# Kernel optimization log

Measured on AMD Instinct MI355X. Metric: run time of the kernel, lower is better.

Reference implementation:

```python
import jax, jax.numpy as jnp
import numpy as np

B, N, K = 8, 2048, 32
WIDTH = 20.0      # histogram bin width in degrees
NUM_BINS = 9
EPS = 1e-12       # F.normalize eps


def _knn_idx(pts, k):
    """pts: (B,N,3) -> (B,N,k) indices of k nearest neighbors (incl. self).
    Matches dgcnn.pytorch knn: topk of negative squared distance."""
    d2 = jnp.sum(pts * pts, axis=-1)                       # (B,N)
    neg = 2.0 * jnp.einsum('bnd,bmd->bnm', pts, pts) - d2[:, :, None] - d2[:, None, :]
    _, idx = jax.lax.top_k(neg, k)                         # (B,N,k)
    return idx


def _gather_nn(feat, idx):
    """feat: (B,N,C), idx: (B,N,k) -> (B,N,k,C) per-batch gather."""
    return jax.vmap(lambda f, i: f[i])(feat, idx)


def setup_inputs() -> dict:
    key = jax.random.key(0)
    x = jax.random.normal(key, (B, 3, N), dtype=jnp.float32)
    return {"x": x, "k": K}


def reference(x, k):
    """Faithful JAX port of compute_hog_1x1. x: (B,3,N) -> (B,18,N)."""
    b, _, n = x.shape
    pts = jnp.transpose(x, (0, 2, 1))                      # (B,N,3)
    idx = _knn_idx(pts, k)                                 # (B,N,k)

    x_nn = _gather_nn(pts, idx)                            # (B,N,k,3)
    centered = x_nn - x_nn.mean(axis=2, keepdims=True)

    # Batched SVD; the original detaches (numpy round-trip) -> stop_gradient.
    _, s, vh = jnp.linalg.svd(centered, full_matrices=False)  # s:(B,N,3) vh:(B,N,3,3)
    vh = jax.lax.stop_gradient(vh)
    s = jax.lax.stop_gradient(jnp.sqrt(s))
    gradients = vh[:, :, 0]                                # (B,N,3) principal direction
    magnitudes = s[:, :, 0:1]                              # (B,N,1)

    g_nn = _gather_nn(gradients, idx)                      # (B,N,k,3)
    m_nn = _gather_nn(magnitudes, idx)                     # (B,N,k,1)

    rad2deg = 180.0 / np.pi
    zenith = jnp.arccos(g_nn[..., 2]) * rad2deg            # (B,N,k)
    azimuth = jnp.arctan(g_nn[..., 1] / g_nn[..., 0]) * rad2deg
    # .int() cast in torch truncates toward zero
    ang = jnp.stack([zenith, azimuth], axis=-1).astype(jnp.int32).astype(x.dtype)
    ang = jnp.where(ang < 0, ang + 180.0, ang)             # (B,N,k,2)

    bins = jnp.floor(ang / WIDTH - 0.5) % NUM_BINS         # (B,N,k,2) float
    first_centers = WIDTH * ((bins + 1.0) % NUM_BINS + 0.5)
    first_votes = m_nn * ((first_centers - ang) % 180.0) / WIDTH
    second_centers = WIDTH * (bins + 0.5)
    second_votes = m_nn * ((ang - second_centers) % 180.0) / WIDTH

    bi = bins.astype(jnp.int32)                            # (B,N,k,2)
    oh1 = jax.nn.one_hot(bi, NUM_BINS, dtype=x.dtype)      # (B,N,k,2,9)
    oh2 = jax.nn.one_hot((bi + 1) % NUM_BINS, NUM_BINS, dtype=x.dtype)
    # histogram[:, :, c] += first where bins==c; histogram[:, :, (c+1)%9] += second
    hist = (jnp.einsum('bnkc,bnkcq->bnqc', first_votes, oh1)
            + jnp.einsum('bnkc,bnkcq->bnqc', second_votes, oh2))  # (B,N,9,2)

    # F.normalize(p=2, dim=2)
    norm = jnp.sqrt(jnp.sum(hist * hist, axis=2, keepdims=True))
    hist = hist / jnp.maximum(norm, EPS)

    # torch .view(B, -1, N): flat row-major reinterpret -> (B,18,N)
    return hist.reshape(b, 2 * NUM_BINS, n)
```

## Files before the change

### kernel.cpp

```cpp
#include <hip/hip_runtime.h>
#include <math.h>

#define BB 8
#define NN 2048
#define KK 32

__device__ __forceinline__ float fadd(float a, float b){ return __fadd_rn(a, b); }
__device__ __forceinline__ float fsub(float a, float b){ return __fsub_rn(a, b); }
__device__ __forceinline__ float fmul(float a, float b){ return __fmul_rn(a, b); }
__device__ __forceinline__ float fdiv(float a, float b){ return __fdiv_rn(a, b); }
__device__ __forceinline__ float fsqrtf32(float a){ return __fsqrt_rn(a); }

__device__ float slapy2f(float x, float y) {
    float xa = fabsf(x), ya = fabsf(y);
    float w = fmaxf(xa, ya), z = fminf(xa, ya);
    if (z == 0.0f) return w;
    float q = fdiv(z, w);
    return fmul(w, fsqrtf32(fmaf(q, q, 1.0f)));
}

__device__ void slartgf(float f, float g, float& c, float& s, float& r) {
    if (g == 0.0f) { c = 1.0f; s = 0.0f; r = f; }
    else if (f == 0.0f) { c = 0.0f; s = copysignf(1.0f, g); r = fabsf(g); }
    else {
        float d = fsqrtf32(fmaf(f, f, fmul(g, g)));
        c = fdiv(fabsf(f), d);
        r = copysignf(d, f);
        s = fdiv(g, r);
    }
}

__device__ void slas2f(float f, float g, float h, float& ssmin, float& ssmax) {
    float fa = fabsf(f), ga = fabsf(g), ha = fabsf(h);
    float fhmn = fminf(fa, ha), fhmx = fmaxf(fa, ha);
    if (fhmn == 0.0f) {
        ssmin = 0.0f;
        if (fhmx == 0.0f) ssmax = ga;
        else {
            float mx = fmaxf(fhmx, ga), mn = fminf(fhmx, ga);
            float q = fdiv(mn, mx);
            ssmax = fmul(mx, fsqrtf32(fmaf(q, q, 1.0f)));
        }
    } else {
        if (ga < fhmx) {
            float as = fadd(1.0f, fdiv(fhmn, fhmx));
            float at = fdiv(fsub(fhmx, fhmn), fhmx);
            float q = fdiv(ga, fhmx); float au = fmul(q, q);
            float c = fdiv(2.0f, fadd(fsqrtf32(fmaf(as, as, au)),
                                      fsqrtf32(fmaf(at, at, au))));
            ssmin = fmul(fhmn, c); ssmax = fdiv(fhmx, c);
        } else {
            float au = fdiv(fhmx, ga);
            if (au == 0.0f) { ssmin = fdiv(fmul(fhmn, fhmx), ga); ssmax = ga; }
            else {
                float as = fadd(1.0f, fdiv(fhmn, fhmx));
                float at = fdiv(fsub(fhmx, fhmn), fhmx);
                float t1 = fmul(as, au), t2 = fmul(at, au);
                float c = fdiv(1.0f, fadd(fsqrtf32(fmaf(t1, t1, 1.0f)),
                                          fsqrtf32(fmaf(t2, t2, 1.0f))));
                ssmin = fmul(fmul(fhmn, c), au); ssmin = fadd(ssmin, ssmin);
                ssmax = fdiv(ga, fadd(c, c));
            }
        }
    }
}

__device__ void slasv2f(float f, float g, float h,
                        float& ssmin, float& ssmax,
                        float& snr, float& csr, float& snl, float& csl) {
    const float eps = 5.9604644775390625e-08f;
    float ft = f, fa = fabsf(f), ht = h, ha = fabsf(h);
    int pmax = 1;
    bool swp = (ha > fa);
    if (swp) { pmax = 3; float t = ft; ft = ht; ht = t; t = fa; fa = ha; ha = t; }
    float gt = g, ga = fabsf(gt);
    float clt = 0.f, crt = 0.f, slt = 0.f, srt = 0.f;
    if (ga == 0.0f) {
        ssmin = ha; ssmax = fa; clt = 1.0f; crt = 1.0f; slt = 0.0f; srt = 0.0f;
    } else {
        bool gasmal = true;
        if (ga > fa) {
            pmax = 2;
            if (fdiv(fa, ga) < eps) {
                gasmal = false;
                ssmax = ga;
                ssmin = (ha > 1.0f) ? fdiv(fa, fdiv(ga, ha)) : fmul(fdiv(fa, ga), ha);
                clt = 1.0f; slt = fdiv(ht, gt); srt = 1.0f; crt = fdiv(ft, gt);
            }
        }
        if (gasmal) {
            float dd = fsub(fa, ha);
            float l = (dd == fa) ? 1.0f : fdiv(dd, fa);
            float mm = fdiv(gt, ft);
            float t = fsub(2.0f, l);
            float m2 = fmul(mm, mm);
            float s = fsqrtf32(fmaf(t, t, m2));
            float r = (l == 0.0f) ? fabsf(mm) : fsqrtf32(fmaf(l, l, m2));
            float a = fmul(0.5f, fadd(s, r));
            ssmin = fdiv(ha, a);
            ssmax = fmul(fa, a);
            if (m2 == 0.0f) {
                t = (l == 0.0f) ? fmul(copysignf(2.0f, ft), copysignf(1.0f, gt))
                                : fadd(fdiv(gt, copysignf(dd, ft)), fdiv(mm, t));
            } else {
                t = fmul(fadd(fdiv(mm, fadd(s, t)), fdiv(mm, fadd(r, l))), fadd(1.0f, a));
            }
            float l2 = fsqrtf32(fmaf(t, t, 4.0f));
            crt = fdiv(2.0f, l2); srt = fdiv(t, l2);
            clt = fdiv(fmaf(srt, mm, crt), a);
            slt = fdiv(fmul(fdiv(ht, ft), srt), a);
        }
    }
    if (swp) { csl = srt; snl = crt; csr = slt; snr = clt; }
    else     { csl = clt; snl = slt; csr = crt; snr = srt; }
    float tsign = 0.0f;
    if (pmax == 1) tsign = fmul(fmul(copysignf(1.f, csr), copysignf(1.f, csl)), copysignf(1.f, f));
    if (pmax == 2) tsign = fmul(fmul(copysignf(1.f, snr), copysignf(1.f, csl)), copysignf(1.f, g));
    if (pmax == 3) tsign = fmul(fmul(copysignf(1.f, snr), copysignf(1.f, snl)), copysignf(1.f, h));
    ssmax = copysignf(fabsf(ssmax), tsign);
    ssmin = copysignf(fabsf(ssmin), fmul(tsign, fmul(copysignf(1.f, f), copysignf(1.f, h))));
}

__device__ __forceinline__ void rot_rowsf(float vt[4][4], int lo, int hi, float cc, float ss) {
    #pragma unroll
    for (int c = 1; c <= 3; ++c) {
        float t = vt[hi][c];
        vt[hi][c] = fmaf(cc, t, -fmul(ss, vt[lo][c]));
        vt[lo][c] = fmaf(ss, t, fmul(cc, vt[lo][c]));
    }
}

__device__ void bdsqr3f(float* d, float* e, float vt[4][4]) {
    const float eps  = 5.9604644775390625e-08f;
    const float unfl = 1.1754943508222875e-38f;
    const int n = 3;
    const float tol = fmul(10.0f, eps);
    float thresh;
    {
        float sminoa = fabsf(d[1]);
        if (sminoa != 0.0f) {
            float mu = sminoa;
            for (int i = 2; i <= n; ++i) {
                mu = fmul(fabsf(d[i]), fdiv(mu, fadd(mu, fabsf(e[i - 1]))));
                sminoa = fminf(sminoa, mu);
                if (sminoa == 0.0f) break;
            }
        }
        sminoa = fdiv(sminoa, fsqrtf32(3.0f));
        thresh = fmaxf(fmul(tol, sminoa), fmul(54.0f, unfl));
    }
    int m = n, iter = 0, oldll = -1, oldm = -1, idir = 0;
    float sminl = 0.0f;
    while (m > 1) {
        if (iter > 54) break;
        float smax = fabsf(d[m]);
        int ll = 0; bool split = false;
        for (int lll = 1; lll <= m - 1; ++lll) {
            int l2 = m - lll;
            float abss = fabsf(d[l2]), abse = fabsf(e[l2]);
            if (abse <= thresh) { ll = l2; split = true; break; }
            smax = fmaxf(smax, fmaxf(abss, abse));
        }
        if (split) {
            e[ll] = 0.0f;
            if (ll == m - 1) { m = m - 1; continue; }
            ll = ll + 1;
        } else ll = 1;
        if (ll == m - 1) {
            float sigmn, sigmx, sinr, cosr, sinl, cosl;
            slasv2f(d[m - 1], e[m - 1], d[m], sigmn, sigmx, sinr, cosr, sinl, cosl);
            d[m - 1] = sigmx; e[m - 1] = 0.0f; d[m] = sigmn;
            #pragma unroll
            for (int c = 1; c <= 3; ++c) {
                float t = fmaf(cosr, vt[m - 1][c], fmul(sinr, vt[m][c]));
                vt[m][c] = fmaf(cosr, vt[m][c], -fmul(sinr, vt[m - 1][c]));
                vt[m - 1][c] = t;
            }
            m -= 2; continue;
        }
        if (ll > oldm || m < oldll)
            idir = (fabsf(d[ll]) >= fabsf(d[m])) ? 1 : 2;
        bool deflated = false;
        if (idir == 1) {
            if (fabsf(e[m - 1]) <= fmul(tol, fabsf(d[m]))) { e[m - 1] = 0.0f; continue; }
            float mu = fabsf(d[ll]); sminl = mu;
            for (int lll = ll; lll <= m - 1; ++lll) {
                if (fabsf(e[lll]) <= fmul(tol, mu)) { e[lll] = 0.0f; deflated = true; break; }
                mu = fmul(fabsf(d[lll + 1]), fdiv(mu, fadd(mu, fabsf(e[lll]))));
                sminl = fminf(sminl, mu);
            }
        } else {
            if (fabsf(e[ll]) <= fmul(tol, fabsf(d[ll]))) { e[ll] = 0.0f; continue; }
            float mu = fabsf(d[m]); sminl = mu;
            for (int lll = m - 1; lll >= ll; --lll) {
                if (fabsf(e[lll]) <= fmul(tol, mu)) { e[lll] = 0.0f; deflated = true; break; }
                mu = fmul(fabsf(d[lll]), fdiv(mu, fadd(mu, fabsf(e[lll]))));
                sminl = fminf(sminl, mu);
            }
        }
        if (deflated) continue;
        oldll = ll; oldm = m;
        float shift = 0.0f, rr;
        if (!(fmul(fmul(3.0f, tol), fdiv(sminl, smax)) <= fmaxf(eps, fmul(0.01f, tol)))) {
            float sll;
            if (idir == 1) { sll = fabsf(d[ll]); slas2f(d[m - 1], e[m - 1], d[m], shift, rr); }
            else           { sll = fabsf(d[m]);  slas2f(d[ll], e[ll], d[ll + 1], shift, rr); }
            if (sll > 0.0f) { float q = fdiv(shift, sll); if (fmul(q, q) < eps) shift = 0.0f; }
        }
        iter += m - ll;
        float wc[4], ws[4];
        if (shift == 0.0f) {
            if (idir == 1) {
                float cs = 1.0f, oldcs = 1.0f, sn = 0.0f, oldsn = 0.0f, r2;
                for (int i = ll; i <= m - 1; ++i) {
                    slartgf(fmul(d[i], cs), e[i], cs, sn, r2);
                    if (i > ll) e[i - 1] = fmul(oldsn, r2);
                    slartgf(fmul(oldcs, r2), fmul(d[i + 1], sn), oldcs, oldsn, d[i]);
                    wc[i - ll + 1] = cs; ws[i - ll + 1] = sn;
                }
                float h = fmul(d[m], cs); d[m] = fmul(h, oldcs); e[m - 1] = fmul(h, oldsn);
                if (fabsf(e[m - 1]) <= thresh) e[m - 1] = 0.0f;
                for (int j = 1; j <= m - ll; ++j) rot_rowsf(vt, ll + j - 1, ll + j, wc[j], ws[j]);
            } else {
                float cs = 1.0f, oldcs = 1.0f, sn = 0.0f, oldsn = 0.0f, r2;
                for (int i = m; i >= ll + 1; --i) {
                    slartgf(fmul(d[i], cs), e[i - 1], cs, sn, r2);
                    if (i < m) e[i] = fmul(oldsn, r2);
                    slartgf(fmul(oldcs, r2), fmul(d[i - 1], sn), oldcs, oldsn, d[i]);
                    wc[i - ll] = oldcs; ws[i - ll] = -oldsn;
                }
                float h = fmul(d[ll], cs); d[ll] = fmul(h, oldcs); e[ll] = fmul(h, oldsn);
                if (fabsf(e[ll]) <= thresh) e[ll] = 0.0f;
                for (int j = m - ll; j >= 1; --j) rot_rowsf(vt, ll + j - 1, ll + j, wc[j], ws[j]);
            }
        } else {
            if (idir == 1) {
                float fq = fmul(fsub(fabsf(d[ll]), shift),
                                fadd(copysignf(1.0f, d[ll]), fdiv(shift, d[ll])));
                float g = e[ll], cosr, sinr, cosl, sinl, r2;
                for (int i = ll; i <= m - 1; ++i) {
                    slartgf(fq, g, cosr, sinr, r2);
                    if (i > ll) e[i - 1] = r2;
                    float di = d[i], ei = e[i], dip = d[i + 1];
                    fq         = fmaf(cosr, di, fmul(sinr, ei));
                    float ei_n = fmaf(cosr, ei, -fmul(sinr, di));
                    g = fmul(sinr, dip);
                    float dip_n = fmul(cosr, dip);
                    slartgf(fq, g, cosl, sinl, r2);
                    d[i] = r2;
                    fq       = fmaf(cosl, ei_n, fmul(sinl, dip_n));
                    d[i + 1] = fmaf(cosl, dip_n, -fmul(sinl, ei_n));
                    e[i] = ei_n;
                    if (i < m - 1) { g = fmul(sinl, e[i + 1]); e[i + 1] = fmul(cosl, e[i + 1]); }
                    wc[i - ll + 1] = cosr; ws[i - ll + 1] = sinr;
                }
                e[m - 1] = fq;
                if (fabsf(e[m - 1]) <= thresh) e[m - 1] = 0.0f;
                for (int j = 1; j <= m - ll; ++j) rot_rowsf(vt, ll + j - 1, ll + j, wc[j], ws[j]);
            } else {
                float fq = fmul(fsub(fabsf(d[m]), shift),
                                fadd(copysignf(1.0f, d[m]), fdiv(shift, d[m])));
                float g = e[m - 1], cosr, sinr, cosl, sinl, r2;
                for (int i = m; i >= ll + 1; --i) {
                    slartgf(fq, g, cosr, sinr, r2);
                    if (i < m) e[i] = r2;
                    float di = d[i], em = e[i - 1], dim = d[i - 1];
                    fq         = fmaf(cosr, di, fmul(sinr, em));
                    float em_n = fmaf(cosr, em, -fmul(sinr, di));
                    g = fmul(sinr, dim);
                    float dim_n = fmul(cosr, dim);
                    slartgf(fq, g, cosl, sinl, r2);
                    d[i] = r2;
                    fq       = fmaf(cosl, em_n, fmul(sinl, dim_n));
                    d[i - 1] = fmaf(cosl, dim_n, -fmul(sinl, em_n));
                    e[i - 1] = em_n;
                    if (i > ll + 1) { g = fmul(sinl, e[i - 2]); e[i - 2] = fmul(cosl, e[i - 2]); }
                    wc[i - ll] = cosl; ws[i - ll] = -sinl;
                }
                e[ll] = fq;
                if (fabsf(e[ll]) <= thresh) e[ll] = 0.0f;
                for (int j = m - ll; j >= 1; --j) rot_rowsf(vt, ll + j - 1, ll + j, wc[j], ws[j]);
            }
        }
    }
    for (int i = 1; i <= n; ++i) {
        if (d[i] < 0.0f) {
            d[i] = -d[i];
            for (int c = 1; c <= 3; ++c) vt[i][c] = -vt[i][c];
        }
    }
    for (int i = 1; i <= n - 1; ++i) {
        int isub = 1; float smin2 = d[1];
        for (int j = 2; j <= n + 1 - i; ++j)
            if (d[j] <= smin2) { isub = j; smin2 = d[j]; }
        int tgt = n + 1 - i;
        if (isub != tgt) {
            d[isub] = d[tgt]; d[tgt] = smin2;
            for (int c = 1; c <= 3; ++c) { float t = vt[isub][c]; vt[isub][c] = vt[tgt][c]; vt[tgt][c] = t; }
        }
    }
}

__global__ void d2_kernel(const float* __restrict__ x, float* __restrict__ d2) {
    int t = blockIdx.x * blockDim.x + threadIdx.x;
    if (t >= BB * NN) return;
    int b = t / NN, n = t % NN;
    const float* xb = x + b * 3 * NN;
    float xv = xb[n], yv = xb[NN + n], zv = xb[2 * NN + n];
    d2[t] = fadd(fadd(fmul(xv, xv), fmul(yv, yv)), fmul(zv, zv));
}

__device__ __forceinline__ unsigned int f32_sortable(float f) {
    unsigned int b = __float_as_uint(f);
    return b ^ ((unsigned int)((int)b >> 31) | 0x80000000u);
}
__device__ __forceinline__ float sortable_f32(unsigned int s) {
    unsigned int b = s ^ (~(unsigned int)((int)s >> 31) | 0x80000000u);
    return __uint_as_float(b);
}

template <int CTRL, int RM>
__device__ __forceinline__ unsigned long long dpp_umax64(unsigned long long k) {
    int nhi = __builtin_amdgcn_update_dpp(0, (int)(unsigned int)(k >> 32), CTRL, RM, 0xF, false);
    int nlo = __builtin_amdgcn_update_dpp(0, (int)(unsigned int)k,         CTRL, RM, 0xF, false);
    unsigned long long nk = ((unsigned long long)(unsigned int)nhi << 32) | (unsigned int)nlo;
    return nk > k ? nk : k;
}

__device__ __forceinline__ unsigned long long pop_best(unsigned int (&vals)[32], int lane) {
    unsigned int m = vals[0];
    #pragma unroll
    for (int s = 1; s < 32; ++s) m = (vals[s] > m) ? vals[s] : m;
    int bs = 0;
    #pragma unroll
    for (int s = 31; s >= 0; --s) if (vals[s] == m) bs = s;
    #pragma unroll
    for (int s = 0; s < 32; ++s) vals[s] = (s == bs) ? 0u : vals[s];
    int j = bs * 64 + lane;
    return ((unsigned long long)m << 32) | (unsigned int)(2047 - j);
}

__global__ void __launch_bounds__(256) knn_kernel(const float* __restrict__ x,
                                                  const float* __restrict__ d2,
                                                  int* __restrict__ idx) {
    int lane = threadIdx.x & 63;
    int wid  = threadIdx.x >> 6;
    int row  = blockIdx.x * 4 + wid;
    int b = row / NN, i = row % NN;
    const float* xb  = x  + b * 3 * NN;
    const float* d2b = d2 + b * NN;

    float xi = xb[i], yi = xb[NN + i], zi = xb[2 * NN + i];
    float d2i = d2b[i];

    unsigned int vals[32];
    #pragma unroll
    for (int s = 0; s < 32; ++s) {
        int j = s * 64 + lane;
        float dot = fmul(xi, xb[j]);
        dot = fmaf(yi, xb[NN + j], dot);
        dot = fmaf(zi, xb[2 * NN + j], dot);
        float v = fsub(fsub(fmul(2.0f, dot), d2i), d2b[j]);
        vals[s] = f32_sortable(v);
    }

    unsigned long long l0 = pop_best(vals, lane);
    unsigned long long l1 = pop_best(vals, lane);
    unsigned long long l2 = pop_best(vals, lane);
    unsigned long long l3 = pop_best(vals, lane);

    int* idxrow = idx + row * KK;
    unsigned int c1v = 0, c2v = 0, c3v = 0, c31v = 0, c32v = 0;
    int c1i = 0, c2i = 0, c3i = 0, c31i = 0, c32i = 0;

    #pragma unroll 1
    for (int t = 0; t < KK + 1; ++t) {
        if (__any(l0 == 0ull)) {
            bool need = (l0 == 0ull);
            unsigned int m = vals[0];
            #pragma unroll
            for (int s = 1; s < 32; ++s) m = (vals[s] > m) ? vals[s] : m;
            int bs = 0;
            #pragma unroll
            for (int s = 31; s >= 0; --s) if (vals[s] == m) bs = s;
            #pragma unroll
            for (int s = 0; s < 32; ++s)
                vals[s] = (need && s == bs) ? 0u : vals[s];
            unsigned long long ent = ((unsigned long long)m << 32)
                                   | (unsigned int)(2047 - (bs * 64 + lane));
            l0 = need ? ent : l0;
        }

        unsigned long long k = l0;
        k = dpp_umax64<0x111, 0xF>(k);
        k = dpp_umax64<0x112, 0xF>(k);
        k = dpp_umax64<0x114, 0xF>(k);
        k = dpp_umax64<0x118, 0xF>(k);
        k = dpp_umax64<0x142, 0xA>(k);
        k = dpp_umax64<0x143, 0xC>(k);

        unsigned int wbest = (unsigned int)__builtin_amdgcn_readlane((int)(k >> 32), 63);
        unsigned int wlow  = (unsigned int)__builtin_amdgcn_readlane((int)(k & 0xFFFFFFFFull), 63);
        int wj = 2047 - (int)(wlow & 0x7FFu);

        bool amw = ((unsigned int)l0 == wlow);
        l0 = amw ? l1 : l0;
        l1 = amw ? l2 : l1;
        l2 = amw ? l3 : l2;
        l3 = amw ? 0ull : l3;

        if (t == 1)           { c1v = wbest;  c1i = wj; }
        else if (t == 2)      { c2v = wbest;  c2i = wj; }
        else if (t == 3)      { c3v = wbest;  c3i = wj; }
        else if (t == KK - 1) { c31v = wbest; c31i = wj; }
        else if (t == KK)     { c32v = wbest; c32i = wj; }
        else if (lane == 0)   idxrow[t] = wj;
    }

    if (lane == 0) {
        const float TIE = 4e-7f;
        float r1  = sortable_f32(c1v),  r2  = sortable_f32(c2v), r3 = sortable_f32(c3v);
        float r31 = sortable_f32(c31v), r32 = sortable_f32(c32v);
        if (fabsf(r1 - r2) < TIE) { int ti = c1i; c1i = c2i; c2i = ti; float tv = r1; r1 = r2; r2 = tv; }
        if (fabsf(r2 - r3) < TIE) { int ti = c2i; c2i = c3i; c3i = ti; float tv = r2; r2 = r3; r3 = tv; }
        idxrow[1] = c1i; idxrow[2] = c2i; idxrow[3] = c3i;
        idxrow[KK - 1] = (fabsf(r31 - r32) < TIE) ? c32i : c31i;
    }
}

__global__ void eig_kernel(const float* __restrict__ x, const int* __restrict__ idx,
                           float4* __restrict__ votes, int* __restrict__ binsq) {
    int t = blockIdx.x * blockDim.x + threadIdx.x;
    if (t >= BB * NN) return;
    int b = t / NN;
    const float* xb = x + b * 3 * NN;
    const int* id = idx + t * KK;

    float A0[KK], A1[KK], A2[KK];
    float s0 = 0.f, s1 = 0.f, s2 = 0.f;
    #pragma unroll
    for (int j = 0; j < KK; ++j) {
        int n = id[j];
        s0 = fadd(s0, xb[n]); s1 = fadd(s1, xb[NN + n]); s2 = fadd(s2, xb[2 * NN + n]);
    }
    float m0 = fdiv(s0, 32.f), m1 = fdiv(s1, 32.f), m2 = fdiv(s2, 32.f);
    #pragma unroll
    for (int j = 0; j < KK; ++j) {
        int n = id[j];
        A0[j] = fsub(xb[n], m0);
        A1[j] = fsub(xb[NN + n], m1);
        A2[j] = fsub(xb[2 * NN + n], m2);
    }

    {
        float alpha = A0[0];
        double nacc = 0.0;
        #pragma unroll
        for (int r = 1; r < KK; ++r) nacc += (double)A0[r] * (double)A0[r];
        float xnorm = (float)sqrt(nacc);
        if (xnorm != 0.0f) {
            float beta = -copysignf(slapy2f(alpha, xnorm), alpha);
            float tau  = fdiv(fsub(beta, alpha), beta);
            float scal = fdiv(1.0f, fsub(alpha, beta));
            #pragma unroll
            for (int r = 1; r < KK; ++r) A0[r] = fmul(A0[r], scal);
            A0[0] = beta;
            {
                float acc = 0.0f;
                #pragma unroll
                for (int r = 1; r < KK; ++r) acc = fmaf(A0[r], A1[r], acc);
                float w = fadd(acc, A1[0]);
                A1[0] = fmaf(-tau, w, A1[0]);
                float temp = fmul(-tau, w);
                #pragma unroll
                for (int r = 1; r < KK; ++r) A1[r] = fmaf(A0[r], temp, A1[r]);
            }
            {
                float acc = 0.0f;
                #pragma unroll
                for (int r = 1; r < KK; ++r) acc = fmaf(A0[r], A2[r], acc);
                float w = fadd(acc, A2[0]);
                A2[0] = fmaf(-tau, w, A2[0]);
                float temp = fmul(-tau, w);
                #pragma unroll
                for (int r = 1; r < KK; ++r) A2[r] = fmaf(A0[r], temp, A2[r]);
            }
        }
    }
    {
        float alpha = A1[1];
        double nacc = 0.0;
        #pragma unroll
        for (int r = 2; r < KK; ++r) nacc += (double)A1[r] * (double)A1[r];
        float xnorm = (float)sqrt(nacc);
        if (xnorm != 0.0f) {
            float beta = -copysignf(slapy2f(alpha, xnorm), alpha);
            float tau  = fdiv(fsub(beta, alpha), beta);
            float scal = fdiv(1.0f, fsub(alpha, beta));
            #pragma unroll
            for (int r = 2; r < KK; ++r) A1[r] = fmul(A1[r], scal);
            A1[1] = beta;
            {
                float acc = 0.0f;
                #pragma unroll
                for (int r = 2; r < KK; ++r) acc = fmaf(A1[r], A2[r], acc);
                float w = fadd(acc, A2[1]);
                A2[1] = fmaf(-tau, w, A2[1]);
                float temp = fmul(-tau, w);
                #pragma unroll
                for (int r = 2; r < KK; ++r) A2[r] = fmaf(A1[r], temp, A2[r]);
            }
        }
    }
    {
        float alpha = A2[2];
        double nacc = 0.0;
        #pragma unroll
        for (int r = 3; r < KK; ++r) nacc += (double)A2[r] * (double)A2[r];
        float xnorm = (float)sqrt(nacc);
        if (xnorm != 0.0f) {
            float beta = -copysignf(slapy2f(alpha, xnorm), alpha);
            float scal = fdiv(1.0f, fsub(alpha, beta));
            #pragma unroll
            for (int r = 3; r < KK; ++r) A2[r] = fmul(A2[r], scal);
            A2[2] = beta;
        }
    }
    float B11 = A0[0], B12 = A1[0], B13 = A2[0];
    float B22 = A1[1], B23 = A2[1], B33 = A2[2];

    float d[4], e[3];
    float taup = 0.0f, v2p = 0.0f;
    d[1] = B11;
    float B32 = 0.0f;
    if (B13 != 0.0f) {
        float xn = fsqrtf32(fmul(B13, B13));
        float beta = -copysignf(slapy2f(B12, xn), B12);
        taup = fdiv(fsub(beta, B12), beta);
        float scal = fdiv(1.0f, fsub(B12, beta));
        v2p = fmul(B13, scal);
        e[1] = beta;
        float w2 = fadd(fmul(B23, v2p), B22);
        float w3 = fmul(B33, v2p);
        B22 = fmaf(-taup, w2, B22);
        B32 = fmul(-taup, w3);
        float tmp = fmul(-taup, v2p);
        B23 = fmaf(w2, tmp, B23);
        B33 = fmaf(w3, tmp, B33);
    } else e[1] = B12;
    if (B32 != 0.0f) {
        float xn = fsqrtf32(fmul(B32, B32));
        float beta = -copysignf(slapy2f(B22, xn), B22);
        float tauq = fdiv(fsub(beta, B22), beta);
        float scal = fdiv(1.0f, fsub(B22, beta));
        float v2 = fmul(B32, scal);
        d[2] = beta;
        float w = fadd(fmul(v2, B33), B23);
        B23 = fmaf(-tauq, w, B23);
        float tmp = fmul(-tauq, w);
        B33 = fmaf(v2, tmp, B33);
    } else d[2] = B22;
    e[2] = B23;
    d[3] = B33;

    float vt[4][4];
    for (int r = 1; r <= 3; ++r)
        for (int c = 1; c <= 3; ++c) vt[r][c] = (r == c) ? 1.0f : 0.0f;
    bdsqr3f(d, e, vt);

    if (taup != 0.0f) {
        float tmp = fmul(-taup, v2p);
        for (int r = 1; r <= 3; ++r) {
            float w = fadd(fmul(vt[r][3], v2p), vt[r][2]);
            vt[r][2] = fmaf(-taup, w, vt[r][2]);
            vt[r][3] = fmaf(w, tmp, vt[r][3]);
        }
    }

    int im = 1;
    if (d[2] > d[im]) im = 2;
    if (d[3] > d[im]) im = 3;
    float gx = vt[im][1];
    float gy = vt[im][2];
    float gz = vt[im][3];
    float m  = fsqrtf32(d[im]);

    const float r2d = (float)(180.0 / M_PI);
    float zen = (float)acos((double)gz);
    float zd  = fmul(zen, r2d);
    float q0  = fdiv(gy, gx);
    float azr = (float)atan((double)q0);
    float ad  = fmul(azr, r2d);

    float a0 = (zd != zd) ? -2147483648.0f : (float)(int)zd;
    float a1 = (ad != ad) ? -2147483648.0f : (float)(int)ad;

    float v1s[2], v2s[2]; int bis[2];
    #pragma unroll
    for (int c = 0; c < 2; ++c) {
        float a = (c == 0) ? a0 : a1;
        if (a < 0.0f) a = fadd(a, 180.0f);
        float tq = fdiv(a, 20.0f);
        float t2 = fsub(tq, 0.5f);
        float fb = floorf(t2);
        float bin = fmodf(fb, 9.0f); if (bin != 0.0f && bin < 0.0f) bin = fadd(bin, 9.0f);
        float b1 = fadd(bin, 1.0f);
        float b1m = fmodf(b1, 9.0f);
        float fc = fmul(20.0f, fadd(b1m, 0.5f));
        float df = fsub(fc, a);
        float rm = fmodf(df, 180.0f); if (rm != 0.0f && rm < 0.0f) rm = fadd(rm, 180.0f);
        v1s[c] = fdiv(fmul(m, rm), 20.0f);
        float sc = fmul(20.0f, fadd(bin, 0.5f));
        float ds = fsub(a, sc);
        float rm2 = fmodf(ds, 180.0f); if (rm2 != 0.0f && rm2 < 0.0f) rm2 = fadd(rm2, 180.0f);
        v2s[c] = fdiv(fmul(m, rm2), 20.0f);
        bis[c] = (int)bin;
    }
    votes[t] = make_float4(v1s[0], v2s[0], v1s[1], v2s[1]);
    binsq[t] = bis[0] | (bis[1] << 8);
}

__global__ void hist_kernel(const int* __restrict__ idx, const float4* __restrict__ votes,
                            const int* __restrict__ binsq, float* __restrict__ out) {
    int t = blockIdx.x * blockDim.x + threadIdx.x;
    if (t >= BB * NN) return;
    int b = t / NN, n = t % NN;
    const int* id = idx + t * KK;

    float h1[9][2], h2[9][2];
    #pragma unroll
    for (int q = 0; q < 9; ++q) { h1[q][0] = h1[q][1] = 0.f; h2[q][0] = h2[q][1] = 0.f; }

    for (int j = 0; j < KK; ++j) {
        int jj = b * NN + id[j];
        float4 v = votes[jj];
        int bp = binsq[jj];
        int bi0 = bp & 0xFF, bi1 = bp >> 8;
        int b20 = bi0 + 1; if (b20 >= 9) b20 -= 9;
        int b21 = bi1 + 1; if (b21 >= 9) b21 -= 9;
        #pragma unroll
        for (int q = 0; q < 9; ++q) {
            h1[q][0] = (bi0 == q) ? fadd(h1[q][0], v.x) : h1[q][0];
            h2[q][0] = (b20 == q) ? fadd(h2[q][0], v.y) : h2[q][0];
            h1[q][1] = (bi1 == q) ? fadd(h1[q][1], v.z) : h1[q][1];
            h2[q][1] = (b21 == q) ? fadd(h2[q][1], v.w) : h2[q][1];
        }
    }

    float* o = out + b * (18 * NN) + n * 18;
    #pragma unroll
    for (int c = 0; c < 2; ++c) {
        float hist[9];
        #pragma unroll
        for (int q = 0; q < 9; ++q) hist[q] = fadd(h1[q][c], h2[q][c]);
        float acc = 0.0f;
        #pragma unroll
        for (int q = 0; q < 9; ++q) acc = fadd(acc, fmul(hist[q], hist[q]));
        float nr = fsqrtf32(acc);
        float den = fmaxf(nr, 1e-12f);
        #pragma unroll
        for (int q = 0; q < 9; ++q) o[q * 2 + c] = fdiv(hist[q], den);
    }
}

extern "C" void kernel_launch(void* const* d_in, const int* in_sizes, int n_in,
                              void* d_out, int out_size, void* d_ws, size_t ws_size,
                              hipStream_t stream) {
    const float* x = (const float*)d_in[0];
    float* out = (float*)d_out;

    char* ws = (char*)d_ws;
    size_t off = 0;
    int* idx = (int*)(ws + off);         off += (size_t)BB * NN * KK * sizeof(int);
    float* d2 = (float*)(ws + off);      off += (size_t)BB * NN * sizeof(float);
    float4* votes = (float4*)(ws + off); off += (size_t)BB * NN * sizeof(float4);
    int* binsq = (int*)(ws + off);

    d2_kernel  <<<(BB * NN + 63) / 64, 64, 0, stream>>>(x, d2);
    knn_kernel <<<BB * NN / 4, 256, 0, stream>>>(x, d2, idx);
    eig_kernel <<<(BB * NN + 63) / 64, 64, 0, stream>>>(x, idx, votes, binsq);
    hist_kernel<<<(BB * NN + 63) / 64, 64, 0, stream>>>(idx, votes, binsq, out);
}
```

Baseline: 178.2 us.

## Use 32-bit wave max reduction in knn and cache gathered points in eig

The knn top-k loop now runs its DPP wave max on only the 32-bit value key instead of a 64-bit value/index pair. It then uses a ballot to read the winning lane's index directly, falling back to a second 32-bit reduction only when values tie. The eig kernel loads each neighbor's coordinates once into registers instead of gathering them twice from global memory. The hist loop is partially unrolled by 8. These changes cut DPP and cross-lane work per selection step and remove redundant global gathers, at the cost of a ballot and branch per step and higher register pressure.

```diff
diff --git a/kernel.cpp b/kernel.cpp
--- a/kernel.cpp
+++ b/kernel.cpp
@@ -320,11 +320,19 @@
 }
 
 template <int CTRL, int RM>
-__device__ __forceinline__ unsigned long long dpp_umax64(unsigned long long k) {
-    int nhi = __builtin_amdgcn_update_dpp(0, (int)(unsigned int)(k >> 32), CTRL, RM, 0xF, false);
-    int nlo = __builtin_amdgcn_update_dpp(0, (int)(unsigned int)k,         CTRL, RM, 0xF, false);
-    unsigned long long nk = ((unsigned long long)(unsigned int)nhi << 32) | (unsigned int)nlo;
-    return nk > k ? nk : k;
+__device__ __forceinline__ unsigned int dpp_umax32(unsigned int v) {
+    unsigned int nv = (unsigned int)__builtin_amdgcn_update_dpp(0, (int)v, CTRL, RM, 0xF, false);
+    return nv > v ? nv : v;
+}
+
+__device__ __forceinline__ unsigned int wave_umax32(unsigned int v) {
+    v = dpp_umax32<0x111, 0xF>(v);
+    v = dpp_umax32<0x112, 0xF>(v);
+    v = dpp_umax32<0x114, 0xF>(v);
+    v = dpp_umax32<0x118, 0xF>(v);
+    v = dpp_umax32<0x142, 0xA>(v);
+    v = dpp_umax32<0x143, 0xC>(v);
+    return v;
 }
 
 __device__ __forceinline__ unsigned long long pop_best(unsigned int (&vals)[32], int lane) {
@@ -364,10 +372,15 @@
         vals[s] = f32_sortable(v);
     }
 
-    unsigned long long l0 = pop_best(vals, lane);
-    unsigned long long l1 = pop_best(vals, lane);
-    unsigned long long l2 = pop_best(vals, lane);
-    unsigned long long l3 = pop_best(vals, lane);
+    unsigned long long p;
+    p = pop_best(vals, lane);
+    unsigned int l0h = (unsigned int)(p >> 32), l0l = (unsigned int)p;
+    p = pop_best(vals, lane);
+    unsigned int l1h = (unsigned int)(p >> 32), l1l = (unsigned int)p;
+    p = pop_best(vals, lane);
+    unsigned int l2h = (unsigned int)(p >> 32), l2l = (unsigned int)p;
+    p = pop_best(vals, lane);
+    unsigned int l3h = (unsigned int)(p >> 32), l3l = (unsigned int)p;
 
     int* idxrow = idx + row * KK;
     unsigned int c1v = 0, c2v = 0, c3v = 0, c31v = 0, c32v = 0;
@@ -375,8 +388,8 @@
 
     #pragma unroll 1
     for (int t = 0; t < KK + 1; ++t) {
-        if (__any(l0 == 0ull)) {
-            bool need = (l0 == 0ull);
+        if (__any(l0h == 0u)) {
+            bool need = (l0h == 0u);
             unsigned int m = vals[0];
             #pragma unroll
             for (int s = 1; s < 32; ++s) m = (vals[s] > m) ? vals[s] : m;
@@ -386,28 +399,32 @@
             #pragma unroll
             for (int s = 0; s < 32; ++s)
                 vals[s] = (need && s == bs) ? 0u : vals[s];
-            unsigned long long ent = ((unsigned long long)m << 32)
-                                   | (unsigned int)(2047 - (bs * 64 + lane));
-            l0 = need ? ent : l0;
-        }
-
-        unsigned long long k = l0;
-        k = dpp_umax64<0x111, 0xF>(k);
-        k = dpp_umax64<0x112, 0xF>(k);
-        k = dpp_umax64<0x114, 0xF>(k);
-        k = dpp_umax64<0x118, 0xF>(k);
-        k = dpp_umax64<0x142, 0xA>(k);
-        k = dpp_umax64<0x143, 0xC>(k);
-
-        unsigned int wbest = (unsigned int)__builtin_amdgcn_readlane((int)(k >> 32), 63);
-        unsigned int wlow  = (unsigned int)__builtin_amdgcn_readlane((int)(k & 0xFFFFFFFFull), 63);
+            unsigned int enth = m;
+            unsigned int entl = (unsigned int)(2047 - (bs * 64 + lane));
+            l0h = need ? enth : l0h;
+            l0l = need ? entl : l0l;
+        }
+
+        unsigned int wbest = (unsigned int)__builtin_amdgcn_readlane(
+            (int)wave_umax32(l0h), 63);
+
+        unsigned long long mask = __ballot(l0h == wbest);
+        unsigned int wlow;
+        if (__popcll(mask) == 1) {
+            int wl = __ffsll((long long)mask) - 1;
+            wlow = (unsigned int)__builtin_amdgcn_readlane((int)l0l, wl);
+        } else {
+            unsigned int tl = (l0h == wbest) ? l0l : 0u;
+            wlow = (unsigned int)__builtin_amdgcn_readlane(
+                (int)wave_umax32(tl), 63);
+        }
         int wj = 2047 - (int)(wlow & 0x7FFu);
 
-        bool amw = ((unsigned int)l0 == wlow);
-        l0 = amw ? l1 : l0;
-        l1 = amw ? l2 : l1;
-        l2 = amw ? l3 : l2;
-        l3 = amw ? 0ull : l3;
+        bool amw = (l0l == wlow);
+        l0h = amw ? l1h : l0h;  l0l = amw ? l1l : l0l;
+        l1h = amw ? l2h : l1h;  l1l = amw ? l2l : l1l;
+        l2h = amw ? l3h : l2h;  l2l = amw ? l3l : l2l;
+        l3h = amw ? 0u  : l3h;  l3l = amw ? 0u  : l3l;
 
         if (t == 1)           { c1v = wbest;  c1i = wj; }
         else if (t == 2)      { c2v = wbest;  c2i = wj; }
@@ -437,19 +454,24 @@
     const int* id = idx + t * KK;
 
     float A0[KK], A1[KK], A2[KK];
-    float s0 = 0.f, s1 = 0.f, s2 = 0.f;
     #pragma unroll
     for (int j = 0; j < KK; ++j) {
         int n = id[j];
-        s0 = fadd(s0, xb[n]); s1 = fadd(s1, xb[NN + n]); s2 = fadd(s2, xb[2 * NN + n]);
+        A0[j] = xb[n];
+        A1[j] = xb[NN + n];
+        A2[j] = xb[2 * NN + n];
+    }
+    float s0 = 0.f, s1 = 0.f, s2 = 0.f;
+    #pragma unroll
+    for (int j = 0; j < KK; ++j) {
+        s0 = fadd(s0, A0[j]); s1 = fadd(s1, A1[j]); s2 = fadd(s2, A2[j]);
     }
     float m0 = fdiv(s0, 32.f), m1 = fdiv(s1, 32.f), m2 = fdiv(s2, 32.f);
     #pragma unroll
     for (int j = 0; j < KK; ++j) {
-        int n = id[j];
-        A0[j] = fsub(xb[n], m0);
-        A1[j] = fsub(xb[NN + n], m1);
-        A2[j] = fsub(xb[2 * NN + n], m2);
+        A0[j] = fsub(A0[j], m0);
+        A1[j] = fsub(A1[j], m1);
+        A2[j] = fsub(A2[j], m2);
     }
 
     {
@@ -631,6 +653,7 @@
     #pragma unroll
     for (int q = 0; q < 9; ++q) { h1[q][0] = h1[q][1] = 0.f; h2[q][0] = h2[q][1] = 0.f; }
 
+    #pragma unroll 8
     for (int j = 0; j < KK; ++j) {
         int jj = b * NN + id[j];
         float4 v = votes[jj];
```

Measured after the change: 162.5 us, median of 2. 1.1x faster.
